# Performance work log

Hardware: AMD Instinct MI355X
Metric: run time of the kernel (lower is better)

Reference implementation:

```python
import jax, jax.numpy as jnp
import numpy as np

N = 100000
E = 1600000
D = 128


def setup_inputs() -> dict:
    key = jax.random.key(0)
    ks = jax.random.split(key, 8)
    x = jax.random.normal(ks[0], (N, D), dtype=jnp.float32)
    edge_index = jax.random.randint(ks[1], (2, E), 0, N, dtype=jnp.int64)
    # Xavier-uniform linear weights, zero-ish biases (PyTorch default bias is uniform; keep small random)
    def xavier(k, fan_in, fan_out):
        limit = float(np.sqrt(6.0 / (fan_in + fan_out)))
        return jax.random.uniform(k, (fan_out, fan_in), minval=-limit, maxval=limit, dtype=jnp.float32)
    W1 = xavier(ks[2], D, D); b1 = jnp.zeros((D,), jnp.float32)
    W2 = xavier(ks[3], D, D); b2 = jnp.zeros((D,), jnp.float32)
    W3 = xavier(ks[4], D, D); b3 = jnp.zeros((D,), jnp.float32)
    return {"x": x, "edge_index": edge_index, "W1": W1, "b1": b1,
            "W2": W2, "b2": b2, "W3": W3, "b3": b3}


def reference(x, edge_index, W1, b1, W2, b2, W3, b3):
    n = x.shape[0]
    loop = jnp.arange(n, dtype=edge_index.dtype)
    row = jnp.concatenate([edge_index[0], loop])  # source (x_j index)
    col = jnp.concatenate([edge_index[1], loop])  # target (aggregation index)
    # degree over row after self-loops; every node appears at least once
    deg = jax.ops.segment_sum(jnp.ones_like(row, dtype=x.dtype), row, num_segments=n)
    dis = deg ** -0.5
    norm = dis[row] * dis[col]  # [E+N]

    def gconv(h, W, b):
        h = h @ W.T + b                      # linear projection [N, D]
        msg = norm[:, None] * h[row]         # gather + elementwise norm [E+N, D]
        return jax.ops.segment_sum(msg, col, num_segments=n)  # scatter-add

    h = jax.nn.relu(gconv(x, W1, b1))
    h = jax.nn.relu(gconv(h, W2, b2))
    h = jax.nn.relu(gconv(h, W3, b3))
    return h
```

## Files before the change

kernel.cpp:

```cpp
#include <hip/hip_runtime.h>
#include <hip/hip_fp16.h>

#define THREADS 256
#define ELL 64
#define RSIZE 32768
#define RS_F 16384
#define NSLICE 64

typedef _Float16 f16x8 __attribute__((ext_vector_type(8)));
typedef float f32x4 __attribute__((ext_vector_type(4)));

__device__ inline uint2 pack_half4(float4 v) {
    __half2 a = __floats2half2_rn(v.x, v.y);
    __half2 b = __floats2half2_rn(v.z, v.w);
    uint2 o;
    o.x = *reinterpret_cast<unsigned int*>(&a);
    o.y = *reinterpret_cast<unsigned int*>(&b);
    return o;
}
__device__ inline float4 unpack_half4(uint2 v) {
    __half2 a = *reinterpret_cast<__half2*>(&v.x);
    __half2 b = *reinterpret_cast<__half2*>(&v.y);
    float2 f0 = __half22float2(a);
    float2 f1 = __half22float2(b);
    return make_float4(f0.x, f0.y, f1.x, f1.y);
}


__global__ void preinit_kernel(const int* __restrict__ ei, int* __restrict__ flag,
                               int* __restrict__ csr, int n) {
    int i = blockIdx.x * blockDim.x + threadIdx.x;
    if (i == 0) {
        int nz = 0;
        for (int k = 1; k < 256; k += 2) nz |= ei[k];
        *flag = (nz == 0) ? 1 : 0;
    }
    if (i < n) csr[(size_t)i * ELL] = i;
}

__global__ __launch_bounds__(THREADS) void fused_pre_kernel(
    const int* __restrict__ ei, const int* __restrict__ flag,
    int* __restrict__ ghist, int* __restrict__ ghistT,
    const float4* __restrict__ x, uint2* __restrict__ h16,
    const float* __restrict__ w0, const float* __restrict__ w1,
    const float* __restrict__ w2, _Float16* __restrict__ wfbuf,
    int eN, int n, int nA, int nC) {
    __shared__ unsigned int lh[RSIZE / 4];
    const int bid = blockIdx.x;
    const int tid = threadIdx.x;

    if (bid < 2 * nA) {
        const bool tgt = (bid >= nA);
        const int b = tgt ? bid - nA : bid;
        const int g = b / NSLICE, s = b % NSLICE;
        int* gout = tgt ? ghistT : ghist;
        for (int i = tid; i < RSIZE / 4; i += THREADS) lh[i] = 0;
        __syncthreads();
        const int lo = (int)((long long)eN * s / NSLICE);
        const int hi = (int)((long long)eN * (s + 1) / NSLICE);
        const int rbase = g * RSIZE;
        const int off = tgt ? eN : 0;
        if (*flag) {
            const long long* e64 = (const long long*)ei;
            for (int idx = lo + tid; idx < hi; idx += THREADS) {
                unsigned int local = (unsigned int)((int)e64[off + idx] - rbase);
                if (local < RSIZE)
                    atomicAdd(&lh[local >> 2], 1u << ((local & 3) << 3));
            }
        } else {
            for (int idx = lo + tid; idx < hi; idx += THREADS) {
                unsigned int local = (unsigned int)(ei[off + idx] - rbase);
                if (local < RSIZE)
                    atomicAdd(&lh[local >> 2], 1u << ((local & 3) << 3));
            }
        }
        __syncthreads();
        for (int i = tid; i < RSIZE; i += THREADS) {
            int node = rbase + i;
            if (node < n)
                gout[(size_t)s * n + node] =
                    (int)((lh[i >> 2] >> ((i & 3) << 3)) & 0xFFu);
        }
    } else if (bid < 2 * nA + nC) {
        const int total = n * 32;
        for (int i = (bid - 2 * nA) * THREADS + tid; i < total; i += nC * THREADS)
            h16[i] = pack_half4(x[i]);
    } else {
        const int i = (bid - 2 * nA - nC) * THREADS + tid;
        if (i < 3 * 8 * 4 * 64) {
            int lane = i & 63;
            int kt = (i >> 6) & 3;
            int nt = (i >> 8) & 7;
            int l  = i >> 11;
            const float* w = (l == 0) ? w0 : (l == 1) ? w1 : w2;
            int o  = nt * 16 + (lane & 15);
            int kb = kt * 32 + (lane >> 4) * 8;
            _Float16* dst = wfbuf + (size_t)i * 8;
#pragma unroll
            for (int j = 0; j < 8; ++j) dst[j] = (_Float16)w[o * 128 + kb + j];
        }
    }
}

__global__ void dis_scanT_kernel(const int* __restrict__ ghist, int* __restrict__ ghistT,
                                 float* __restrict__ dis, int* __restrict__ fill, int n) {
    int i = blockIdx.x * blockDim.x + threadIdx.x;
    if (i >= n) return;
    int deg = 1;
#pragma unroll 8
    for (int s = 0; s < NSLICE; ++s) deg += ghist[(size_t)s * n + i];
    dis[i] = 1.0f / sqrtf((float)deg);
    int running = 1;
    for (int s = 0; s < NSLICE; ++s) {
        size_t idx = (size_t)s * n + i;
        int cnt = ghistT[idx];
        ghistT[idx] = running;
        running += cnt;
    }
    fill[i] = running;
}

__global__ __launch_bounds__(THREADS) void fill2_kernel(
    const int* __restrict__ ei, const int* __restrict__ flag,
    const int* __restrict__ starts, int* __restrict__ csr, int eN, int n) {
    __shared__ unsigned int lcur[RS_F];
    const int s = blockIdx.x % NSLICE;
    const int g = blockIdx.x / NSLICE;
    const int rbase = g * RS_F;
    const int tid = threadIdx.x;
    for (int i = tid; i < RS_F; i += THREADS) {
        int node = rbase + i;
        lcur[i] = (node < n) ? (unsigned int)starts[(size_t)s * n + node] : 0u;
    }
    __syncthreads();
    const int lo = (int)((long long)eN * s / NSLICE);
    const int hi = (int)((long long)eN * (s + 1) / NSLICE);
    if (*flag) {
        const long long* e64 = (const long long*)ei;
        for (int idx = lo + tid; idx < hi; idx += THREADS) {
            int c = (int)e64[eN + idx];
            unsigned int local = (unsigned int)(c - rbase);
            if (local < RS_F) {
                int r = (int)e64[idx];
                unsigned int pos = atomicAdd(&lcur[local], 1u);
                csr[(size_t)c * ELL + pos] = r;
            }
        }
    } else {
        for (int idx = lo + tid; idx < hi; idx += THREADS) {
            int c = ei[eN + idx];
            unsigned int local = (unsigned int)(c - rbase);
            if (local < RS_F) {
                int r = ei[idx];
                unsigned int pos = atomicAdd(&lcur[local], 1u);
                csr[(size_t)c * ELL + pos] = r;
            }
        }
    }
}

__global__ void sumw_kernel(const int* __restrict__ csr, const int* __restrict__ fill,
                            const float* __restrict__ dis, float* __restrict__ sumw,
                            float* __restrict__ w32, int n) {
    int i = blockIdx.x * blockDim.x + threadIdx.x;
    if (i >= n) return;
    int len = fill[i];
    const int base = i * ELL;
    const float dg = dis[i];
    float t = 0.f;
    for (int j = 0; j < len; ++j) {
        float w = dg * dis[csr[base + j]];
        w32[base + j] = w;
        t += w;
    }
    sumw[i] = t;
}


__global__ void agg_kernel(const uint2* __restrict__ h, const int* __restrict__ csr,
                           const int* __restrict__ fill, const float* __restrict__ w32,
                           uint2* __restrict__ out, int n) {
    const int wid = blockIdx.x * (blockDim.x >> 6) + (threadIdx.x >> 6);
    const int lane = threadIdx.x & 63;
    const int half = lane >> 5;
    const int l32 = lane & 31;
    if (wid >= n) return;
    const int len = fill[wid];
    const int base = wid * ELL;

    float4 a0 = make_float4(0.f, 0.f, 0.f, 0.f);
    float4 a1 = make_float4(0.f, 0.f, 0.f, 0.f);
    float4 a2 = make_float4(0.f, 0.f, 0.f, 0.f);
    float4 a3 = make_float4(0.f, 0.f, 0.f, 0.f);
    int j = half;
    for (; j + 6 < len; j += 8) {
        int u0 = csr[base + j];
        int u1 = csr[base + j + 2];
        int u2 = csr[base + j + 4];
        int u3 = csr[base + j + 6];
        float w0 = w32[base + j];
        float w1 = w32[base + j + 2];
        float w2 = w32[base + j + 4];
        float w3 = w32[base + j + 6];
        float4 v0 = unpack_half4(h[(size_t)u0 * 32 + l32]);
        float4 v1 = unpack_half4(h[(size_t)u1 * 32 + l32]);
        float4 v2 = unpack_half4(h[(size_t)u2 * 32 + l32]);
        float4 v3 = unpack_half4(h[(size_t)u3 * 32 + l32]);
        a0.x = fmaf(w0, v0.x, a0.x); a0.y = fmaf(w0, v0.y, a0.y);
        a0.z = fmaf(w0, v0.z, a0.z); a0.w = fmaf(w0, v0.w, a0.w);
        a1.x = fmaf(w1, v1.x, a1.x); a1.y = fmaf(w1, v1.y, a1.y);
        a1.z = fmaf(w1, v1.z, a1.z); a1.w = fmaf(w1, v1.w, a1.w);
        a2.x = fmaf(w2, v2.x, a2.x); a2.y = fmaf(w2, v2.y, a2.y);
        a2.z = fmaf(w2, v2.z, a2.z); a2.w = fmaf(w2, v2.w, a2.w);
        a3.x = fmaf(w3, v3.x, a3.x); a3.y = fmaf(w3, v3.y, a3.y);
        a3.z = fmaf(w3, v3.z, a3.z); a3.w = fmaf(w3, v3.w, a3.w);
    }
    for (; j < len; j += 2) {
        int u = csr[base + j];
        float w = w32[base + j];
        float4 v = unpack_half4(h[(size_t)u * 32 + l32]);
        a0.x = fmaf(w, v.x, a0.x); a0.y = fmaf(w, v.y, a0.y);
        a0.z = fmaf(w, v.z, a0.z); a0.w = fmaf(w, v.w, a0.w);
    }
    a0.x += a1.x + a2.x + a3.x;
    a0.y += a1.y + a2.y + a3.y;
    a0.z += a1.z + a2.z + a3.z;
    a0.w += a1.w + a2.w + a3.w;

    a0.x += __shfl_xor(a0.x, 32, 64);
    a0.y += __shfl_xor(a0.y, 32, 64);
    a0.z += __shfl_xor(a0.z, 32, 64);
    a0.w += __shfl_xor(a0.w, 32, 64);

    if (half == 0) {
        out[(size_t)wid * 32 + l32] = pack_half4(a0);
    }
}

template <bool OUT16>
__global__ __launch_bounds__(THREADS) void lin_mfma_kernel(
    const _Float16* __restrict__ a16, const _Float16* __restrict__ wfrag,
    const float* __restrict__ bias, const float* __restrict__ sumw,
    float* __restrict__ outf, _Float16* __restrict__ outh, int n) {
    const int lane = threadIdx.x & 63;
    const int g = lane >> 4;
    const int m15 = lane & 15;
    const int wavesPerBlock = blockDim.x >> 6;
    const int wave = blockIdx.x * wavesPerBlock + (threadIdx.x >> 6);
    const int nwaves = gridDim.x * wavesPerBlock;

    f16x8 wf[8][4];
#pragma unroll
    for (int nt = 0; nt < 8; ++nt)
#pragma unroll
        for (int kt = 0; kt < 4; ++kt)
            wf[nt][kt] = *reinterpret_cast<const f16x8*>(
                wfrag + ((size_t)((nt * 4 + kt) * 64 + lane)) * 8);

    const int ntiles = (n + 15) >> 4;
    for (int t = wave; t < ntiles; t += nwaves) {
        const int myrow = t * 16 + m15;
        const int rr = (myrow < n) ? myrow : (n - 1);
        const _Float16* arow = a16 + (size_t)rr * 128 + g * 8;
        f16x8 af[4];
#pragma unroll
        for (int kt = 0; kt < 4; ++kt)
            af[kt] = *reinterpret_cast<const f16x8*>(arow + kt * 32);

        f32x4 acc[8];
#pragma unroll
        for (int nt = 0; nt < 8; ++nt) acc[nt] = (f32x4){0.f, 0.f, 0.f, 0.f};
#pragma unroll
        for (int kt = 0; kt < 4; ++kt)
#pragma unroll
            for (int nt = 0; nt < 8; ++nt)
                acc[nt] = __builtin_amdgcn_mfma_f32_16x16x32_f16(
                    wf[nt][kt], af[kt], acc[nt], 0, 0, 0);

        if (myrow < n) {
            const float sw = sumw[myrow];
#pragma unroll
            for (int nt = 0; nt < 8; ++nt) {
                const float4 b4 = *reinterpret_cast<const float4*>(bias + nt * 16 + g * 4);
                float vx = fmaxf(acc[nt][0] + sw * b4.x, 0.f);
                float vy = fmaxf(acc[nt][1] + sw * b4.y, 0.f);
                float vz = fmaxf(acc[nt][2] + sw * b4.z, 0.f);
                float vw = fmaxf(acc[nt][3] + sw * b4.w, 0.f);
                size_t oidx = (size_t)myrow * 128 + nt * 16 + g * 4;
                if (OUT16) {
                    *reinterpret_cast<uint2*>(outh + oidx) =
                        pack_half4(make_float4(vx, vy, vz, vw));
                } else {
                    *reinterpret_cast<float4*>(outf + oidx) =
                        make_float4(vx, vy, vz, vw);
                }
            }
        }
    }
}


extern "C" void kernel_launch(void* const* d_in, const int* in_sizes, int n_in,
                              void* d_out, int out_size, void* d_ws, size_t ws_size,
                              hipStream_t stream) {
    const float* x  = (const float*)d_in[0];
    const int*   ei = (const int*)d_in[1];
    const float* Ws[3] = {(const float*)d_in[2], (const float*)d_in[4], (const float*)d_in[6]};
    const float* bs[3] = {(const float*)d_in[3], (const float*)d_in[5], (const float*)d_in[7]};
    const int n = in_sizes[0] / 128;
    const int e = in_sizes[1] / 2;

    char* ws = (char*)d_ws;
    size_t cur = 0;
    auto alloc = [&](size_t bytes) {
        void* p = ws + cur;
        cur = (cur + bytes + 255) & ~(size_t)255;
        return p;
    };
    uint2*     A16   = (uint2*)alloc((size_t)n * 128 * 2);
    uint2*     H16   = (uint2*)alloc((size_t)n * 128 * 2);
    int*       csr   = (int*)  alloc((size_t)n * ELL * 4);
    float*     w32   = (float*)alloc((size_t)n * ELL * 4);
    int*       ghistT= (int*)  w32;
    int*       ghist = (int*)  alloc((size_t)NSLICE * n * 4);
    int*       fill  = (int*)  alloc((size_t)n * 4);
    float*     dis   = (float*)alloc((size_t)n * 4);
    float*     sumw  = (float*)alloc((size_t)n * 4);
    _Float16*  wf    = (_Float16*)alloc(3 * 8 * 4 * 64 * 8 * 2);
    int*       flag  = (int*)  alloc(4);

    const int nr = (n + RSIZE - 1) / RSIZE;
    const int nA = nr * NSLICE;
    const int nC = 256;
    const int nD = (3 * 8 * 4 * 64 + THREADS - 1) / THREADS;
    const int nrF = (n + RS_F - 1) / RS_F;

    preinit_kernel<<<(n + 255) / 256, 256, 0, stream>>>(ei, flag, csr, n);
    fused_pre_kernel<<<2 * nA + nC + nD, THREADS, 0, stream>>>(
        ei, flag, ghist, ghistT, (const float4*)x, H16,
        Ws[0], Ws[1], Ws[2], wf, e, n, nA, nC);
    dis_scanT_kernel<<<(n + 255) / 256, 256, 0, stream>>>(ghist, ghistT, dis, fill, n);
    fill2_kernel<<<nrF * NSLICE, THREADS, 0, stream>>>(ei, flag, ghistT, csr, e, n);
    sumw_kernel<<<(n + 255) / 256, 256, 0, stream>>>(csr, fill, dis, sumw, w32, n);

    for (int l = 0; l < 3; ++l) {
        agg_kernel<<<(n + 3) / 4, 256, 0, stream>>>(
            H16, csr, fill, w32, A16, n);
        const _Float16* wfl = wf + (size_t)l * 8 * 4 * 64 * 8;
        if (l < 2) {
            lin_mfma_kernel<true><<<512, THREADS, 0, stream>>>(
                (const _Float16*)A16, wfl, bs[l], sumw,
                nullptr, (_Float16*)H16, n);
        } else {
            lin_mfma_kernel<false><<<512, THREADS, 0, stream>>>(
                (const _Float16*)A16, wfl, bs[l], sumw,
                (float*)d_out, nullptr, n);
        }
    }
}
```

Before: 431.9 us.

## Pack fill cursors as bytes in LDS to cover more nodes per block

The CSR fill kernel now keeps four 8-bit per-node cursors in each 32-bit LDS word and updates them with shifted atomic adds. Each block can then cover 65536 nodes instead of 16384, so there are fewer node-range groups and each slice's edge range is rescanned fewer times. Block size goes to 512 threads, and RSIZE (used by the histogram phase) is also doubled. The byte cursors assume every per-node position stays below 256 (ELL is 64), and packing four nodes per word may add LDS atomic contention.

```diff
diff --git a/kernel.cpp b/kernel.cpp
--- a/kernel.cpp
+++ b/kernel.cpp
@@ -3,8 +3,9 @@
 
 #define THREADS 256
 #define ELL 64
-#define RSIZE 32768
-#define RS_F 16384
+#define RSIZE 65536
+#define RS_F 65536
+#define FTHREADS 512
 #define NSLICE 64
 
 typedef _Float16 f16x8 __attribute__((ext_vector_type(8)));
@@ -120,39 +121,49 @@
     fill[i] = running;
 }
 
-__global__ __launch_bounds__(THREADS) void fill2_kernel(
+__global__ __launch_bounds__(FTHREADS) void fill2_kernel(
     const int* __restrict__ ei, const int* __restrict__ flag,
     const int* __restrict__ starts, int* __restrict__ csr, int eN, int n) {
-    __shared__ unsigned int lcur[RS_F];
+    __shared__ unsigned int lcur[RS_F / 4];
     const int s = blockIdx.x % NSLICE;
     const int g = blockIdx.x / NSLICE;
     const int rbase = g * RS_F;
     const int tid = threadIdx.x;
-    for (int i = tid; i < RS_F; i += THREADS) {
-        int node = rbase + i;
-        lcur[i] = (node < n) ? (unsigned int)starts[(size_t)s * n + node] : 0u;
+    const int* st = starts + (size_t)s * n;
+    for (int i = tid; i < RS_F / 4; i += FTHREADS) {
+        int n0 = rbase + i * 4;
+        unsigned int w = 0;
+#pragma unroll
+        for (int k = 0; k < 4; ++k) {
+            int node = n0 + k;
+            unsigned int v = (node < n) ? (unsigned int)st[node] : 0u;
+            w |= (v & 0xFFu) << (k * 8);
+        }
+        lcur[i] = w;
     }
     __syncthreads();
     const int lo = (int)((long long)eN * s / NSLICE);
     const int hi = (int)((long long)eN * (s + 1) / NSLICE);
     if (*flag) {
         const long long* e64 = (const long long*)ei;
-        for (int idx = lo + tid; idx < hi; idx += THREADS) {
+        for (int idx = lo + tid; idx < hi; idx += FTHREADS) {
             int c = (int)e64[eN + idx];
             unsigned int local = (unsigned int)(c - rbase);
             if (local < RS_F) {
                 int r = (int)e64[idx];
-                unsigned int pos = atomicAdd(&lcur[local], 1u);
+                unsigned int old = atomicAdd(&lcur[local >> 2], 1u << ((local & 3) << 3));
+                unsigned int pos = (old >> ((local & 3) << 3)) & 0xFFu;
                 csr[(size_t)c * ELL + pos] = r;
             }
         }
     } else {
-        for (int idx = lo + tid; idx < hi; idx += THREADS) {
+        for (int idx = lo + tid; idx < hi; idx += FTHREADS) {
             int c = ei[eN + idx];
             unsigned int local = (unsigned int)(c - rbase);
             if (local < RS_F) {
                 int r = ei[idx];
-                unsigned int pos = atomicAdd(&lcur[local], 1u);
+                unsigned int old = atomicAdd(&lcur[local >> 2], 1u << ((local & 3) << 3));
+                unsigned int pos = (old >> ((local & 3) << 3)) & 0xFFu;
                 csr[(size_t)c * ELL + pos] = r;
             }
         }
@@ -340,7 +351,7 @@
         ei, flag, ghist, ghistT, (const float4*)x, H16,
         Ws[0], Ws[1], Ws[2], wf, e, n, nA, nC);
     dis_scanT_kernel<<<(n + 255) / 256, 256, 0, stream>>>(ghist, ghistT, dis, fill, n);
-    fill2_kernel<<<nrF * NSLICE, THREADS, 0, stream>>>(ei, flag, ghistT, csr, e, n);
+    fill2_kernel<<<nrF * NSLICE, FTHREADS, 0, stream>>>(ei, flag, ghistT, csr, e, n);
     sumw_kernel<<<(n + 255) / 256, 256, 0, stream>>>(csr, fill, dis, sumw, w32, n);
 
     for (int l = 0; l < 3; ++l) {
```

After: 430.1 us. No clear change (-0.4%).
